# Performance work log

Measured on AMD Instinct MI355X. Metric: run time of the kernel, lower is better.

Reference implementation:

```python
import jax, jax.numpy as jnp
import numpy as np


def _lstm_selu(x, W, U, b):
    """Keras-semantics LSTM with activation='selu', return_sequences=True.
    x: [B, T, F]; W: [F, 4H]; U: [H, 4H]; b: [4H]. Gate order i, f, g, o.
    """
    B = x.shape[0]
    H = U.shape[0]
    # Precompute the input projection for all timesteps (one big GEMM).
    xz = jnp.einsum('btf,fg->btg', x, W) + b  # [B, T, 4H]

    def step(carry, xt):
        h, c = carry
        z = xt + h @ U  # [B, 4H]
        i, f, g, o = jnp.split(z, 4, axis=-1)
        i = jax.nn.sigmoid(i)
        f = jax.nn.sigmoid(f)
        g = jax.nn.selu(g)          # activation='selu' on candidate
        o = jax.nn.sigmoid(o)
        c = f * c + i * g
        h = o * jax.nn.selu(c)      # activation='selu' on cell output
        return (h, c), h

    h0 = jnp.zeros((B, H), x.dtype)
    c0 = jnp.zeros((B, H), x.dtype)
    (_, _), hs = jax.lax.scan(step, (h0, c0), jnp.swapaxes(xz, 0, 1))  # hs: [T, B, H]
    return jnp.swapaxes(hs, 0, 1)  # [B, T, H]


def setup_inputs() -> dict:
    key = jax.random.key(0)
    ks = jax.random.split(key, 6)
    B, T, F, H = 64, 2048, 64, 128
    s_in1 = 1.0 / np.sqrt(F)
    s_rec = 1.0 / np.sqrt(H)
    return {
        'x': jax.random.normal(ks[0], (B, T, F), dtype=jnp.float32),
        'W1': jax.random.normal(ks[1], (F, 4 * H), dtype=jnp.float32) * s_in1,
        'U1': jax.random.normal(ks[2], (H, 4 * H), dtype=jnp.float32) * s_rec,
        'b1': jnp.zeros((4 * H,), dtype=jnp.float32),
        'W2': jax.random.normal(ks[3], (H, 4 * H), dtype=jnp.float32) * s_rec,
        'U2': jax.random.normal(ks[4], (H, 4 * H), dtype=jnp.float32) * s_rec,
        'b2': jnp.zeros((4 * H,), dtype=jnp.float32),
    }


def reference(x, W1, U1, b1, W2, U2, b2):
    h1 = _lstm_selu(x, W1, U1, b1)   # layer 1, return_sequences=True
    h2 = _lstm_selu(h1, W2, U2, b2)  # layer 2 consumes layer-1 sequence
    return h2
```

## Files before the change

### kernel.cpp

```cpp
#include <hip/hip_runtime.h>
#include <hip/hip_bf16.h>

#define BATCH 64
#define SEQT  2048
#define FEAT  64
#define HID   128
#define G4    512
#define CHUNK 16
#define NCHUNK (SEQT / CHUNK)
#define XSP  68
#define H1P  136
#define XZP  516

using short8  = __attribute__((ext_vector_type(8))) short;
using floatx4 = __attribute__((ext_vector_type(4))) float;

__device__ __forceinline__ float sigmoidf_(float x) {
    return __builtin_amdgcn_rcpf(1.0f + __expf(-x));
}
__device__ __forceinline__ float seluf_(float x) {
    const float a = 1.6732632423543772f;
    const float s = 1.0507009873554805f;
    return x > 0.0f ? s * x : s * a * (__expf(x) - 1.0f);
}
__device__ __forceinline__ unsigned short f2bf_(float f) {
    unsigned u = __float_as_uint(f);
    u += 0x7FFFu + ((u >> 16) & 1u);
    return (unsigned short)(u >> 16);
}

__global__ __launch_bounds__(512)
__attribute__((amdgpu_waves_per_eu(2, 2)))
void fused_lstm(const float* __restrict__ x,
                const float* __restrict__ W1,
                const float* __restrict__ U1,
                const float* __restrict__ b1,
                const float* __restrict__ W2,
                const float* __restrict__ U2,
                const float* __restrict__ b2,
                unsigned long long* __restrict__ h1g,
                unsigned* __restrict__ flags,
                float* __restrict__ out) {
    const bool l2  = blockIdx.x >= BATCH;
    const int  b   = l2 ? ((int)blockIdx.x - BATCH) : (int)blockIdx.x;
    const int tid  = threadIdx.x;
    const int w    = tid >> 6;
    const int lane = tid & 63;
    const int c16  = lane & 15;
    const int quad = lane >> 4;
    const int j    = w * 16 + c16;

    __shared__ __align__(16) short hA[2][HID];
    __shared__ __align__(16) float xzbuf[CHUNK * XZP];
    __shared__ __align__(16) float xs[CHUNK * XSP];
    __shared__ __align__(16) short h1c[CHUNK * H1P];
    __shared__ __align__(16) short h1buf[CHUNK * HID];
    __shared__ __align__(16) float hbuf[CHUNK * HID];

    const float* U = l2 ? U2 : U1;
    short8 bfrag[4][4];
#pragma unroll
    for (int g = 0; g < 4; ++g) {
        const float* Ucol = U + (size_t)(g * 128 + j);
#pragma unroll
        for (int kc = 0; kc < 4; ++kc) {
            short8 v;
#pragma unroll
            for (int jj = 0; jj < 8; ++jj) {
                int k = kc * 32 + quad * 8 + jj;
                v[jj] = (short)f2bf_(Ucol[(size_t)k * G4]);
            }
            bfrag[g][kc] = v;
        }
    }

    const float* Wp = l2 ? W2 : W1;
    short8 wfrag[4][4];
#pragma unroll
    for (int g = 0; g < 4; ++g) {
        const float* Wcol = Wp + (size_t)(g * 128 + j);
#pragma unroll
        for (int kc = 0; kc < 4; ++kc) {
            short8 v;
            if (l2 || kc < 2) {
#pragma unroll
                for (int jj = 0; jj < 8; ++jj) {
                    int k = kc * 32 + quad * 8 + jj;
                    v[jj] = (short)f2bf_(Wcol[(size_t)k * G4]);
                }
            } else {
#pragma unroll
                for (int jj = 0; jj < 8; ++jj) v[jj] = 0;
            }
            wfrag[g][kc] = v;
        }
    }
    const float* bb = l2 ? b2 : b1;
    const float4 bias4 = make_float4(bb[j], bb[128 + j], bb[256 + j], bb[384 + j]);

    const float* xb = x + (size_t)b * SEQT * FEAT;
    if (!l2) {
        if (tid < 256) {
            float4 v = ((const float4*)xb)[tid];
            int t = tid >> 4, k4 = (tid & 15) << 2;
            *(float4*)&xs[t * XSP + k4] = v;
        }
    }
    if (tid < HID) hA[0][tid] = 0;
    float cst = 0.0f;
    floatx4 zero4 = {0.f, 0.f, 0.f, 0.f};
    __syncthreads();

    float*              out_b  = out + (size_t)b * SEQT * HID;
    unsigned long long* h1g_b  = h1g + (size_t)b * (SEQT * HID / 4);

    for (int c = 0; c < NCHUNK; ++c) {
        float4 pf;
        if (!l2) {
            if (c + 1 < NCHUNK && tid < 256)
                pf = ((const float4*)(xb + (size_t)(c + 1) * CHUNK * FEAT))[tid];
            short8 axf[2];
#pragma unroll
            for (int kc = 0; kc < 2; ++kc) {
                const float* p = &xs[c16 * XSP + kc * 32 + quad * 8];
                float4 f0 = *(const float4*)p;
                float4 f1 = *(const float4*)(p + 4);
                short8 v;
                v[0] = (short)f2bf_(f0.x); v[1] = (short)f2bf_(f0.y);
                v[2] = (short)f2bf_(f0.z); v[3] = (short)f2bf_(f0.w);
                v[4] = (short)f2bf_(f1.x); v[5] = (short)f2bf_(f1.y);
                v[6] = (short)f2bf_(f1.z); v[7] = (short)f2bf_(f1.w);
                axf[kc] = v;
            }
            floatx4 acc1[4];
#pragma unroll
            for (int g = 0; g < 4; ++g)
                acc1[g] = __builtin_amdgcn_mfma_f32_16x16x32_bf16(axf[0], wfrag[g][0], zero4, 0, 0, 0);
#pragma unroll
            for (int g = 0; g < 4; ++g)
                acc1[g] = __builtin_amdgcn_mfma_f32_16x16x32_bf16(axf[1], wfrag[g][1], acc1[g], 0, 0, 0);
#pragma unroll
            for (int r = 0; r < 4; ++r) {
                int s = quad * 4 + r;
                *(float4*)&xzbuf[s * XZP + j * 4] =
                    make_float4(acc1[0][r] + bias4.x, acc1[1][r] + bias4.y,
                                acc1[2][r] + bias4.z, acc1[3][r] + bias4.w);
            }
            __syncthreads();
        } else {
            if (tid == 0) {
                while (__hip_atomic_load(&flags[b], __ATOMIC_RELAXED,
                                         __HIP_MEMORY_SCOPE_AGENT) < (unsigned)(c + 1))
                    __builtin_amdgcn_s_sleep(8);
            }
            __syncthreads();
            {
                unsigned long long hv = __hip_atomic_load(
                    h1g_b + (size_t)c * 512 + tid, __ATOMIC_RELAXED, __HIP_MEMORY_SCOPE_AGENT);
                int t = tid >> 5, kg = tid & 31;
                *(unsigned long long*)&h1c[t * H1P + kg * 4] = hv;
            }
            __syncthreads();

            short8 af2[4];
#pragma unroll
            for (int kc = 0; kc < 4; ++kc)
                af2[kc] = *(const short8*)&h1c[c16 * H1P + kc * 32 + quad * 8];
            floatx4 acc2[4];
#pragma unroll
            for (int g = 0; g < 4; ++g)
                acc2[g] = __builtin_amdgcn_mfma_f32_16x16x32_bf16(af2[0], wfrag[g][0], zero4, 0, 0, 0);
#pragma unroll
            for (int kc = 1; kc < 4; ++kc)
#pragma unroll
                for (int g = 0; g < 4; ++g)
                    acc2[g] = __builtin_amdgcn_mfma_f32_16x16x32_bf16(af2[kc], wfrag[g][kc], acc2[g], 0, 0, 0);
#pragma unroll
            for (int r = 0; r < 4; ++r) {
                int s = quad * 4 + r;
                *(float4*)&xzbuf[s * XZP + j * 4] =
                    make_float4(acc2[0][r] + bias4.x, acc2[1][r] + bias4.y,
                                acc2[2][r] + bias4.z, acc2[3][r] + bias4.w);
            }
            __syncthreads();
        }

#pragma unroll 2
        for (int s = 0; s < CHUNK; ++s) {
            const short* hb = &hA[s & 1][0];
            short8 af[4];
#pragma unroll
            for (int kc = 0; kc < 4; ++kc)
                af[kc] = *(const short8*)&hb[kc * 32 + quad * 8];

            float4 xq = *(const float4*)&xzbuf[s * XZP + j * 4];

            floatx4 acc[4];
#pragma unroll
            for (int g = 0; g < 4; ++g)
                acc[g] = __builtin_amdgcn_mfma_f32_16x16x32_bf16(af[0], bfrag[g][0], zero4, 0, 0, 0);
#pragma unroll
            for (int kc = 1; kc < 4; ++kc)
#pragma unroll
                for (int g = 0; g < 4; ++g)
                    acc[g] = __builtin_amdgcn_mfma_f32_16x16x32_bf16(af[kc], bfrag[g][kc], acc[g], 0, 0, 0);

            float zi = acc[0][0] + xq.x;
            float zf = acc[1][0] + xq.y;
            float zg = acc[2][0] + xq.z;
            float zo = acc[3][0] + xq.w;
            float ig = sigmoidf_(zi);
            float fg = sigmoidf_(zf);
            float gg = seluf_(zg);
            float og = sigmoidf_(zo);
            cst = fg * cst + ig * gg;
            float h = og * seluf_(cst);

            if (lane < 16) {
                unsigned short hb16 = f2bf_(h);
                hA[(s + 1) & 1][j] = (short)hb16;
                if (l2) hbuf[s * HID + j] = h;
                else    h1buf[s * HID + j] = (short)hb16;
            }
            __syncthreads();
        }

        if (!l2) {
            unsigned long long hv = *(const unsigned long long*)&h1buf[tid * 4];
            __hip_atomic_store(h1g_b + (size_t)c * 512 + tid, hv,
                               __ATOMIC_RELAXED, __HIP_MEMORY_SCOPE_AGENT);
            if (c + 1 < NCHUNK && tid < 256) {
                int t = tid >> 4, k4 = (tid & 15) << 2;
                *(float4*)&xs[t * XSP + k4] = pf;
            }
            __syncthreads();
            if (tid == 0)
                __hip_atomic_store(&flags[b], (unsigned)(c + 1),
                                   __ATOMIC_RELAXED, __HIP_MEMORY_SCOPE_AGENT);
        } else {
            float4 hv = *(const float4*)&hbuf[tid * 4];
            *(float4*)&out_b[(size_t)c * CHUNK * HID + tid * 4] = hv;
        }
    }
}

extern "C" void kernel_launch(void* const* d_in, const int* in_sizes, int n_in,
                              void* d_out, int out_size, void* d_ws, size_t ws_size,
                              hipStream_t stream) {
    const float* x  = (const float*)d_in[0];
    const float* W1 = (const float*)d_in[1];
    const float* U1 = (const float*)d_in[2];
    const float* b1 = (const float*)d_in[3];
    const float* W2 = (const float*)d_in[4];
    const float* U2 = (const float*)d_in[5];
    const float* b2 = (const float*)d_in[6];
    float* out = (float*)d_out;

    const size_t BT       = (size_t)BATCH * SEQT;
    const size_t H1_BYTES = BT * HID * 2;

    unsigned long long* h1g   = (unsigned long long*)d_ws;
    unsigned*           flags = (unsigned*)((char*)d_ws + H1_BYTES);

    hipMemsetAsync(flags, 0, BATCH * sizeof(unsigned), stream);

    fused_lstm<<<dim3(2 * BATCH), dim3(512), 0, stream>>>(
        x, W1, U1, b1, W2, U2, b2, h1g, flags, out);
}
```

Measured before the change: 1.293 ms.

## Halve block to four waves, each owning two hidden-column groups with split-K MFMA chains

Cuts the workgroup from 8 to 4 waves so each wave computes 32 hidden columns, holding twice the U and W fragments in registers. The recurrent MFMA chain is split into two independent K-halves that are summed afterwards, which shortens the dependent chain and cuts the number of waves joining each per-step barrier. The spin-wait sleep is also shortened. The cost is a much higher register footprint, with possible spills at one wave per EU, and twice the gate math per thread on the serial critical path.

```diff
diff --git a/kernel.cpp b/kernel.cpp
--- a/kernel.cpp
+++ b/kernel.cpp
@@ -29,8 +29,8 @@
     return (unsigned short)(u >> 16);
 }
 
-__global__ __launch_bounds__(512)
-__attribute__((amdgpu_waves_per_eu(2, 2)))
+__global__ __launch_bounds__(256)
+__attribute__((amdgpu_waves_per_eu(1, 1)))
 void fused_lstm(const float* __restrict__ x,
                 const float* __restrict__ W1,
                 const float* __restrict__ U1,
@@ -48,7 +48,8 @@
     const int lane = tid & 63;
     const int c16  = lane & 15;
     const int quad = lane >> 4;
-    const int j    = w * 16 + c16;
+    const int j0   = w * 32 + c16;
+    const int j1   = j0 + 16;
 
     __shared__ __align__(16) short hA[2][HID];
     __shared__ __align__(16) float xzbuf[CHUNK * XZP];
@@ -58,68 +59,68 @@
     __shared__ __align__(16) float hbuf[CHUNK * HID];
 
     const float* U = l2 ? U2 : U1;
-    short8 bfrag[4][4];
-#pragma unroll
-    for (int g = 0; g < 4; ++g) {
-        const float* Ucol = U + (size_t)(g * 128 + j);
-#pragma unroll
-        for (int kc = 0; kc < 4; ++kc) {
-            short8 v;
-#pragma unroll
-            for (int jj = 0; jj < 8; ++jj) {
-                int k = kc * 32 + quad * 8 + jj;
-                v[jj] = (short)f2bf_(Ucol[(size_t)k * G4]);
-            }
-            bfrag[g][kc] = v;
-        }
-    }
-
-    const float* Wp = l2 ? W2 : W1;
-    short8 wfrag[4][4];
-#pragma unroll
-    for (int g = 0; g < 4; ++g) {
-        const float* Wcol = Wp + (size_t)(g * 128 + j);
-#pragma unroll
-        for (int kc = 0; kc < 4; ++kc) {
-            short8 v;
-            if (l2 || kc < 2) {
+    short8 bfrag[4][4][2];
+#pragma unroll
+    for (int g = 0; g < 4; ++g)
+#pragma unroll
+        for (int grp = 0; grp < 2; ++grp) {
+            const float* Ucol = U + (size_t)(g * 128 + w * 32 + grp * 16 + c16);
+#pragma unroll
+            for (int kc = 0; kc < 4; ++kc) {
+                short8 v;
 #pragma unroll
                 for (int jj = 0; jj < 8; ++jj) {
                     int k = kc * 32 + quad * 8 + jj;
-                    v[jj] = (short)f2bf_(Wcol[(size_t)k * G4]);
-                }
-            } else {
-#pragma unroll
-                for (int jj = 0; jj < 8; ++jj) v[jj] = 0;
-            }
-            wfrag[g][kc] = v;
-        }
-    }
+                    v[jj] = (short)f2bf_(Ucol[(size_t)k * G4]);
+                }
+                bfrag[kc][g][grp] = v;
+            }
+        }
+
+    const float* Wp = l2 ? W2 : W1;
+    const int KCW = l2 ? 4 : 2;
+    short8 wfrag[4][4][2];
+#pragma unroll
+    for (int g = 0; g < 4; ++g)
+#pragma unroll
+        for (int grp = 0; grp < 2; ++grp) {
+            const float* Wcol = Wp + (size_t)(g * 128 + w * 32 + grp * 16 + c16);
+#pragma unroll
+            for (int kc = 0; kc < 4; ++kc) {
+                if (kc < KCW) {
+                    short8 v;
+#pragma unroll
+                    for (int jj = 0; jj < 8; ++jj) {
+                        int k = kc * 32 + quad * 8 + jj;
+                        v[jj] = (short)f2bf_(Wcol[(size_t)k * G4]);
+                    }
+                    wfrag[kc][g][grp] = v;
+                }
+            }
+        }
     const float* bb = l2 ? b2 : b1;
-    const float4 bias4 = make_float4(bb[j], bb[128 + j], bb[256 + j], bb[384 + j]);
+    const float4 biasA = make_float4(bb[j0], bb[128 + j0], bb[256 + j0], bb[384 + j0]);
+    const float4 biasB = make_float4(bb[j1], bb[128 + j1], bb[256 + j1], bb[384 + j1]);
 
     const float* xb = x + (size_t)b * SEQT * FEAT;
     if (!l2) {
-        if (tid < 256) {
-            float4 v = ((const float4*)xb)[tid];
-            int t = tid >> 4, k4 = (tid & 15) << 2;
-            *(float4*)&xs[t * XSP + k4] = v;
-        }
+        float4 v = ((const float4*)xb)[tid];
+        *(float4*)&xs[(tid >> 4) * XSP + ((tid & 15) << 2)] = v;
     }
     if (tid < HID) hA[0][tid] = 0;
-    float cst = 0.0f;
+    float cst0 = 0.0f, cst1 = 0.0f;
     floatx4 zero4 = {0.f, 0.f, 0.f, 0.f};
     __syncthreads();
 
-    float*              out_b  = out + (size_t)b * SEQT * HID;
-    unsigned long long* h1g_b  = h1g + (size_t)b * (SEQT * HID / 4);
+    float*              out_b = out + (size_t)b * SEQT * HID;
+    unsigned long long* h1g_b = h1g + (size_t)b * (SEQT * HID / 4);
 
     for (int c = 0; c < NCHUNK; ++c) {
         float4 pf;
         if (!l2) {
-            if (c + 1 < NCHUNK && tid < 256)
+            if (c + 1 < NCHUNK)
                 pf = ((const float4*)(xb + (size_t)(c + 1) * CHUNK * FEAT))[tid];
-            short8 axf[2];
+            short8 ax[2];
 #pragma unroll
             for (int kc = 0; kc < 2; ++kc) {
                 const float* p = &xs[c16 * XSP + kc * 32 + quad * 8];
@@ -130,57 +131,66 @@
                 v[2] = (short)f2bf_(f0.z); v[3] = (short)f2bf_(f0.w);
                 v[4] = (short)f2bf_(f1.x); v[5] = (short)f2bf_(f1.y);
                 v[6] = (short)f2bf_(f1.z); v[7] = (short)f2bf_(f1.w);
-                axf[kc] = v;
-            }
-            floatx4 acc1[4];
+                ax[kc] = v;
+            }
+            floatx4 acc1[4][2];
 #pragma unroll
             for (int g = 0; g < 4; ++g)
-                acc1[g] = __builtin_amdgcn_mfma_f32_16x16x32_bf16(axf[0], wfrag[g][0], zero4, 0, 0, 0);
-#pragma unroll
-            for (int g = 0; g < 4; ++g)
-                acc1[g] = __builtin_amdgcn_mfma_f32_16x16x32_bf16(axf[1], wfrag[g][1], acc1[g], 0, 0, 0);
+#pragma unroll
+                for (int grp = 0; grp < 2; ++grp) {
+                    floatx4 t = __builtin_amdgcn_mfma_f32_16x16x32_bf16(ax[0], wfrag[0][g][grp], zero4, 0, 0, 0);
+                    acc1[g][grp] = __builtin_amdgcn_mfma_f32_16x16x32_bf16(ax[1], wfrag[1][g][grp], t, 0, 0, 0);
+                }
 #pragma unroll
             for (int r = 0; r < 4; ++r) {
-                int s = quad * 4 + r;
-                *(float4*)&xzbuf[s * XZP + j * 4] =
-                    make_float4(acc1[0][r] + bias4.x, acc1[1][r] + bias4.y,
-                                acc1[2][r] + bias4.z, acc1[3][r] + bias4.w);
+                int srow = quad * 4 + r;
+                *(float4*)&xzbuf[srow * XZP + j0 * 4] =
+                    make_float4(acc1[0][0][r] + biasA.x, acc1[1][0][r] + biasA.y,
+                                acc1[2][0][r] + biasA.z, acc1[3][0][r] + biasA.w);
+                *(float4*)&xzbuf[srow * XZP + j1 * 4] =
+                    make_float4(acc1[0][1][r] + biasB.x, acc1[1][1][r] + biasB.y,
+                                acc1[2][1][r] + biasB.z, acc1[3][1][r] + biasB.w);
             }
             __syncthreads();
         } else {
             if (tid == 0) {
                 while (__hip_atomic_load(&flags[b], __ATOMIC_RELAXED,
                                          __HIP_MEMORY_SCOPE_AGENT) < (unsigned)(c + 1))
-                    __builtin_amdgcn_s_sleep(8);
-            }
-            __syncthreads();
-            {
+                    __builtin_amdgcn_s_sleep(2);
+            }
+            __syncthreads();
+#pragma unroll
+            for (int i = 0; i < 2; ++i) {
+                int idx = tid + i * 256;
                 unsigned long long hv = __hip_atomic_load(
-                    h1g_b + (size_t)c * 512 + tid, __ATOMIC_RELAXED, __HIP_MEMORY_SCOPE_AGENT);
-                int t = tid >> 5, kg = tid & 31;
-                *(unsigned long long*)&h1c[t * H1P + kg * 4] = hv;
-            }
-            __syncthreads();
-
-            short8 af2[4];
+                    h1g_b + (size_t)c * 512 + idx, __ATOMIC_RELAXED, __HIP_MEMORY_SCOPE_AGENT);
+                *(unsigned long long*)&h1c[(idx >> 5) * H1P + (idx & 31) * 4] = hv;
+            }
+            __syncthreads();
+
+            short8 ah[4];
 #pragma unroll
             for (int kc = 0; kc < 4; ++kc)
-                af2[kc] = *(const short8*)&h1c[c16 * H1P + kc * 32 + quad * 8];
-            floatx4 acc2[4];
+                ah[kc] = *(const short8*)&h1c[c16 * H1P + kc * 32 + quad * 8];
+            floatx4 acc2[4][2];
 #pragma unroll
             for (int g = 0; g < 4; ++g)
-                acc2[g] = __builtin_amdgcn_mfma_f32_16x16x32_bf16(af2[0], wfrag[g][0], zero4, 0, 0, 0);
-#pragma unroll
-            for (int kc = 1; kc < 4; ++kc)
-#pragma unroll
-                for (int g = 0; g < 4; ++g)
-                    acc2[g] = __builtin_amdgcn_mfma_f32_16x16x32_bf16(af2[kc], wfrag[g][kc], acc2[g], 0, 0, 0);
+#pragma unroll
+                for (int grp = 0; grp < 2; ++grp) {
+                    floatx4 t = __builtin_amdgcn_mfma_f32_16x16x32_bf16(ah[0], wfrag[0][g][grp], zero4, 0, 0, 0);
+                    t = __builtin_amdgcn_mfma_f32_16x16x32_bf16(ah[1], wfrag[1][g][grp], t, 0, 0, 0);
+                    t = __builtin_amdgcn_mfma_f32_16x16x32_bf16(ah[2], wfrag[2][g][grp], t, 0, 0, 0);
+                    acc2[g][grp] = __builtin_amdgcn_mfma_f32_16x16x32_bf16(ah[3], wfrag[3][g][grp], t, 0, 0, 0);
+                }
 #pragma unroll
             for (int r = 0; r < 4; ++r) {
-                int s = quad * 4 + r;
-                *(float4*)&xzbuf[s * XZP + j * 4] =
-                    make_float4(acc2[0][r] + bias4.x, acc2[1][r] + bias4.y,
-                                acc2[2][r] + bias4.z, acc2[3][r] + bias4.w);
+                int srow = quad * 4 + r;
+                *(float4*)&xzbuf[srow * XZP + j0 * 4] =
+                    make_float4(acc2[0][0][r] + biasA.x, acc2[1][0][r] + biasA.y,
+                                acc2[2][0][r] + biasA.z, acc2[3][0][r] + biasA.w);
+                *(float4*)&xzbuf[srow * XZP + j1 * 4] =
+                    make_float4(acc2[0][1][r] + biasB.x, acc2[1][1][r] + biasB.y,
+                                acc2[2][1][r] + biasB.z, acc2[3][1][r] + biasB.w);
             }
             __syncthreads();
         }
@@ -192,54 +202,76 @@
 #pragma unroll
             for (int kc = 0; kc < 4; ++kc)
                 af[kc] = *(const short8*)&hb[kc * 32 + quad * 8];
-
-            float4 xq = *(const float4*)&xzbuf[s * XZP + j * 4];
-
-            floatx4 acc[4];
+            float4 xqA = *(const float4*)&xzbuf[s * XZP + j0 * 4];
+            float4 xqB = *(const float4*)&xzbuf[s * XZP + j1 * 4];
+
+            floatx4 accA[4][2], accB[4][2];
 #pragma unroll
             for (int g = 0; g < 4; ++g)
-                acc[g] = __builtin_amdgcn_mfma_f32_16x16x32_bf16(af[0], bfrag[g][0], zero4, 0, 0, 0);
-#pragma unroll
-            for (int kc = 1; kc < 4; ++kc)
-#pragma unroll
-                for (int g = 0; g < 4; ++g)
-                    acc[g] = __builtin_amdgcn_mfma_f32_16x16x32_bf16(af[kc], bfrag[g][kc], acc[g], 0, 0, 0);
-
-            float zi = acc[0][0] + xq.x;
-            float zf = acc[1][0] + xq.y;
-            float zg = acc[2][0] + xq.z;
-            float zo = acc[3][0] + xq.w;
-            float ig = sigmoidf_(zi);
-            float fg = sigmoidf_(zf);
-            float gg = seluf_(zg);
-            float og = sigmoidf_(zo);
-            cst = fg * cst + ig * gg;
-            float h = og * seluf_(cst);
-
-            if (lane < 16) {
-                unsigned short hb16 = f2bf_(h);
-                hA[(s + 1) & 1][j] = (short)hb16;
-                if (l2) hbuf[s * HID + j] = h;
-                else    h1buf[s * HID + j] = (short)hb16;
+#pragma unroll
+                for (int grp = 0; grp < 2; ++grp) {
+                    floatx4 t0 = __builtin_amdgcn_mfma_f32_16x16x32_bf16(af[0], bfrag[0][g][grp], zero4, 0, 0, 0);
+                    accA[g][grp] = __builtin_amdgcn_mfma_f32_16x16x32_bf16(af[1], bfrag[1][g][grp], t0, 0, 0, 0);
+                    floatx4 t1 = __builtin_amdgcn_mfma_f32_16x16x32_bf16(af[2], bfrag[2][g][grp], zero4, 0, 0, 0);
+                    accB[g][grp] = __builtin_amdgcn_mfma_f32_16x16x32_bf16(af[3], bfrag[3][g][grp], t1, 0, 0, 0);
+                }
+
+            float h0, h1f;
+            unsigned short h0b, h1b;
+            {
+                float zi = accA[0][0][0] + accB[0][0][0] + xqA.x;
+                float zf = accA[1][0][0] + accB[1][0][0] + xqA.y;
+                float zg = accA[2][0][0] + accB[2][0][0] + xqA.z;
+                float zo = accA[3][0][0] + accB[3][0][0] + xqA.w;
+                float ig = sigmoidf_(zi), fg = sigmoidf_(zf);
+                float gg = seluf_(zg),   og = sigmoidf_(zo);
+                cst0 = fg * cst0 + ig * gg;
+                h0 = og * seluf_(cst0);
+                h0b = f2bf_(h0);
+            }
+            {
+                float zi = accA[0][1][0] + accB[0][1][0] + xqB.x;
+                float zf = accA[1][1][0] + accB[1][1][0] + xqB.y;
+                float zg = accA[2][1][0] + accB[2][1][0] + xqB.z;
+                float zo = accA[3][1][0] + accB[3][1][0] + xqB.w;
+                float ig = sigmoidf_(zi), fg = sigmoidf_(zf);
+                float gg = seluf_(zg),   og = sigmoidf_(zo);
+                cst1 = fg * cst1 + ig * gg;
+                h1f = og * seluf_(cst1);
+                h1b = f2bf_(h1f);
+            }
+
+            if (lane < 32) {
+                int col = w * 32 + lane;
+                unsigned short hv = (lane < 16) ? h0b : h1b;
+                hA[(s + 1) & 1][col] = (short)hv;
+                if (l2) hbuf[s * HID + col] = (lane < 16) ? h0 : h1f;
+                else    h1buf[s * HID + col] = (short)hv;
             }
             __syncthreads();
         }
 
         if (!l2) {
-            unsigned long long hv = *(const unsigned long long*)&h1buf[tid * 4];
-            __hip_atomic_store(h1g_b + (size_t)c * 512 + tid, hv,
-                               __ATOMIC_RELAXED, __HIP_MEMORY_SCOPE_AGENT);
-            if (c + 1 < NCHUNK && tid < 256) {
-                int t = tid >> 4, k4 = (tid & 15) << 2;
-                *(float4*)&xs[t * XSP + k4] = pf;
-            }
+#pragma unroll
+            for (int i = 0; i < 2; ++i) {
+                int idx = tid + i * 256;
+                unsigned long long hv = *(const unsigned long long*)&h1buf[idx * 4];
+                __hip_atomic_store(h1g_b + (size_t)c * 512 + idx, hv,
+                                   __ATOMIC_RELAXED, __HIP_MEMORY_SCOPE_AGENT);
+            }
+            if (c + 1 < NCHUNK)
+                *(float4*)&xs[(tid >> 4) * XSP + ((tid & 15) << 2)] = pf;
             __syncthreads();
             if (tid == 0)
                 __hip_atomic_store(&flags[b], (unsigned)(c + 1),
                                    __ATOMIC_RELAXED, __HIP_MEMORY_SCOPE_AGENT);
         } else {
-            float4 hv = *(const float4*)&hbuf[tid * 4];
-            *(float4*)&out_b[(size_t)c * CHUNK * HID + tid * 4] = hv;
+#pragma unroll
+            for (int i = 0; i < 2; ++i) {
+                int idx = tid + i * 256;
+                *(float4*)&out_b[(size_t)c * CHUNK * HID + idx * 4] =
+                    *(const float4*)&hbuf[idx * 4];
+            }
         }
     }
 }
@@ -264,6 +296,6 @@
 
     hipMemsetAsync(flags, 0, BATCH * sizeof(unsigned), stream);
 
-    fused_lstm<<<dim3(2 * BATCH), dim3(512), 0, stream>>>(
+    fused_lstm<<<dim3(2 * BATCH), dim3(256), 0, stream>>>(
         x, W1, U1, b1, W2, U2, b2, h1g, flags, out);
 }
```

New measurement: 1.736 ms. 1.34x slower.

## Fuse both LSTM layers into one 1024-thread block per batch with skewed chunks

Applied to the files above, without the earlier changes.

Rather than running layer-1 and layer-2 in separate blocks that talk through global memory with flag spin-waits, each block now has 16 waves. Waves 0-7 run layer 1 and waves 8-15 run layer 2, one chunk behind, and they hand off h1 through a double-buffered shared-memory tile. Input-projection weights are pre-converted to bf16 fragments by a small prep kernel and read from global memory rather than held in registers, which frees registers for the 1024-thread launch. The intent is to remove the global handoff, the atomics and the polling latency. The cost is that both layers now share one barrier per timestep, layer 2's output is written per step, and only 64 blocks run.

```diff
diff --git a/kernel.cpp b/kernel.cpp
--- a/kernel.cpp
+++ b/kernel.cpp
@@ -15,6 +15,8 @@
 using short8  = __attribute__((ext_vector_type(8))) short;
 using floatx4 = __attribute__((ext_vector_type(4))) float;
 
+#define BAR_LGKM() asm volatile("s_waitcnt lgkmcnt(0)\n\ts_barrier" ::: "memory")
+
 __device__ __forceinline__ float sigmoidf_(float x) {
     return __builtin_amdgcn_rcpf(1.0f + __expf(-x));
 }
@@ -29,35 +31,53 @@
     return (unsigned short)(u >> 16);
 }
 
-__global__ __launch_bounds__(512)
-__attribute__((amdgpu_waves_per_eu(2, 2)))
+__global__ __launch_bounds__(256) void prep_weights(const float* __restrict__ W1,
+                                                    const float* __restrict__ W2,
+                                                    unsigned short* __restrict__ wsf) {
+    int idx = blockIdx.x * 256 + threadIdx.x;
+    int KC, fi, obase;
+    const float* src;
+    if (idx < 4096) { KC = 2; src = W1; fi = idx;        obase = 0; }
+    else            { KC = 4; src = W2; fi = idx - 4096; obase = 4096 * 8; }
+    int g  = fi & 3;
+    int r  = fi >> 2;
+    int kc = r % KC;
+    int p  = r / KC;
+    int q  = p & 3;
+    int j  = p >> 2;
+    short8 v;
+#pragma unroll
+    for (int jj = 0; jj < 8; ++jj)
+        v[jj] = (short)f2bf_(src[(size_t)(kc * 32 + q * 8 + jj) * G4 + g * 128 + j]);
+    *(short8*)&wsf[obase + fi * 8] = v;
+}
+
+__global__ __launch_bounds__(1024)
 void fused_lstm(const float* __restrict__ x,
-                const float* __restrict__ W1,
                 const float* __restrict__ U1,
                 const float* __restrict__ b1,
-                const float* __restrict__ W2,
                 const float* __restrict__ U2,
                 const float* __restrict__ b2,
-                unsigned long long* __restrict__ h1g,
-                unsigned* __restrict__ flags,
+                const unsigned short* __restrict__ wsf,
                 float* __restrict__ out) {
-    const bool l2  = blockIdx.x >= BATCH;
-    const int  b   = l2 ? ((int)blockIdx.x - BATCH) : (int)blockIdx.x;
+    const int  b   = (int)blockIdx.x;
     const int tid  = threadIdx.x;
     const int w    = tid >> 6;
+    const bool l2w = w >= 8;
+    const int  wl  = w & 7;
     const int lane = tid & 63;
     const int c16  = lane & 15;
     const int quad = lane >> 4;
-    const int j    = w * 16 + c16;
-
-    __shared__ __align__(16) short hA[2][HID];
-    __shared__ __align__(16) float xzbuf[CHUNK * XZP];
+    const int j    = wl * 16 + c16;
+
+    __shared__ __align__(16) short hA1[2][HID];
+    __shared__ __align__(16) short hA2[2][HID];
+    __shared__ __align__(16) float xz1[CHUNK * XZP];
+    __shared__ __align__(16) float xz2[CHUNK * XZP];
     __shared__ __align__(16) float xs[CHUNK * XSP];
-    __shared__ __align__(16) short h1c[CHUNK * H1P];
-    __shared__ __align__(16) short h1buf[CHUNK * HID];
-    __shared__ __align__(16) float hbuf[CHUNK * HID];
-
-    const float* U = l2 ? U2 : U1;
+    __shared__ __align__(16) short h1x[2][CHUNK * H1P];
+
+    const float* U = l2w ? U2 : U1;
     short8 bfrag[4][4];
 #pragma unroll
     for (int g = 0; g < 4; ++g) {
@@ -70,177 +90,115 @@
                 int k = kc * 32 + quad * 8 + jj;
                 v[jj] = (short)f2bf_(Ucol[(size_t)k * G4]);
             }
-            bfrag[g][kc] = v;
+            bfrag[kc][g] = v;
         }
     }
-
-    const float* Wp = l2 ? W2 : W1;
-    short8 wfrag[4][4];
-#pragma unroll
-    for (int g = 0; g < 4; ++g) {
-        const float* Wcol = Wp + (size_t)(g * 128 + j);
-#pragma unroll
-        for (int kc = 0; kc < 4; ++kc) {
-            short8 v;
-            if (l2 || kc < 2) {
-#pragma unroll
-                for (int jj = 0; jj < 8; ++jj) {
-                    int k = kc * 32 + quad * 8 + jj;
-                    v[jj] = (short)f2bf_(Wcol[(size_t)k * G4]);
-                }
-            } else {
-#pragma unroll
-                for (int jj = 0; jj < 8; ++jj) v[jj] = 0;
-            }
-            wfrag[g][kc] = v;
-        }
+    const float* bb = l2w ? b2 : b1;
+    const float4 bias4 = make_float4(bb[j], bb[128 + j], bb[256 + j], bb[384 + j]);
+
+    const int KC = l2w ? 4 : 2;
+    const short8* wtb = (const short8*)(wsf + (l2w ? 32768 : 0)
+                                            + (size_t)(j * 4 + quad) * KC * 32);
+
+    const float* xb    = x + (size_t)b * SEQT * FEAT;
+    float*       out_b = out + (size_t)b * SEQT * HID;
+
+    if (!l2w && tid < 256) {
+        float4 v = ((const float4*)xb)[tid];
+        *(float4*)&xs[(tid >> 4) * XSP + ((tid & 15) << 2)] = v;
     }
-    const float* bb = l2 ? b2 : b1;
-    const float4 bias4 = make_float4(bb[j], bb[128 + j], bb[256 + j], bb[384 + j]);
-
-    const float* xb = x + (size_t)b * SEQT * FEAT;
-    if (!l2) {
-        if (tid < 256) {
-            float4 v = ((const float4*)xb)[tid];
-            int t = tid >> 4, k4 = (tid & 15) << 2;
-            *(float4*)&xs[t * XSP + k4] = v;
-        }
-    }
-    if (tid < HID) hA[0][tid] = 0;
+    if (tid < HID) hA1[0][tid] = 0;
+    else if (tid < 2 * HID) hA2[0][tid - HID] = 0;
     float cst = 0.0f;
     floatx4 zero4 = {0.f, 0.f, 0.f, 0.f};
     __syncthreads();
 
-    float*              out_b  = out + (size_t)b * SEQT * HID;
-    unsigned long long* h1g_b  = h1g + (size_t)b * (SEQT * HID / 4);
-
-    for (int c = 0; c < NCHUNK; ++c) {
+    short (*hAp)[HID] = l2w ? hA2 : hA1;
+    float* myxz       = l2w ? xz2 : xz1;
+
+    for (int c = 0; c <= NCHUNK; ++c) {
+        const bool act = l2w ? (c >= 1) : (c < NCHUNK);
         float4 pf;
-        if (!l2) {
-            if (c + 1 < NCHUNK && tid < 256)
-                pf = ((const float4*)(xb + (size_t)(c + 1) * CHUNK * FEAT))[tid];
-            short8 axf[2];
-#pragma unroll
-            for (int kc = 0; kc < 2; ++kc) {
-                const float* p = &xs[c16 * XSP + kc * 32 + quad * 8];
-                float4 f0 = *(const float4*)p;
-                float4 f1 = *(const float4*)(p + 4);
-                short8 v;
-                v[0] = (short)f2bf_(f0.x); v[1] = (short)f2bf_(f0.y);
-                v[2] = (short)f2bf_(f0.z); v[3] = (short)f2bf_(f0.w);
-                v[4] = (short)f2bf_(f1.x); v[5] = (short)f2bf_(f1.y);
-                v[6] = (short)f2bf_(f1.z); v[7] = (short)f2bf_(f1.w);
-                axf[kc] = v;
-            }
-            floatx4 acc1[4];
-#pragma unroll
-            for (int g = 0; g < 4; ++g)
-                acc1[g] = __builtin_amdgcn_mfma_f32_16x16x32_bf16(axf[0], wfrag[g][0], zero4, 0, 0, 0);
-#pragma unroll
-            for (int g = 0; g < 4; ++g)
-                acc1[g] = __builtin_amdgcn_mfma_f32_16x16x32_bf16(axf[1], wfrag[g][1], acc1[g], 0, 0, 0);
+        if (!l2w && c + 1 < NCHUNK && tid < 256)
+            pf = ((const float4*)(xb + (size_t)(c + 1) * CHUNK * FEAT))[tid];
+
+        if (act) {
+            floatx4 accp[4] = {zero4, zero4, zero4, zero4};
+            for (int kc = 0; kc < KC; ++kc) {
+                short8 aop;
+                if (!l2w) {
+                    const float* p = &xs[c16 * XSP + kc * 32 + quad * 8];
+                    float4 f0 = *(const float4*)p;
+                    float4 f1 = *(const float4*)(p + 4);
+                    aop[0] = (short)f2bf_(f0.x); aop[1] = (short)f2bf_(f0.y);
+                    aop[2] = (short)f2bf_(f0.z); aop[3] = (short)f2bf_(f0.w);
+                    aop[4] = (short)f2bf_(f1.x); aop[5] = (short)f2bf_(f1.y);
+                    aop[6] = (short)f2bf_(f1.z); aop[7] = (short)f2bf_(f1.w);
+                } else {
+                    aop = *(const short8*)&h1x[(c + 1) & 1][c16 * H1P + kc * 32 + quad * 8];
+                }
+                short8 w0 = wtb[kc * 4 + 0], w1 = wtb[kc * 4 + 1];
+                short8 w2 = wtb[kc * 4 + 2], w3 = wtb[kc * 4 + 3];
+                accp[0] = __builtin_amdgcn_mfma_f32_16x16x32_bf16(aop, w0, accp[0], 0, 0, 0);
+                accp[1] = __builtin_amdgcn_mfma_f32_16x16x32_bf16(aop, w1, accp[1], 0, 0, 0);
+                accp[2] = __builtin_amdgcn_mfma_f32_16x16x32_bf16(aop, w2, accp[2], 0, 0, 0);
+                accp[3] = __builtin_amdgcn_mfma_f32_16x16x32_bf16(aop, w3, accp[3], 0, 0, 0);
+            }
 #pragma unroll
             for (int r = 0; r < 4; ++r) {
-                int s = quad * 4 + r;
-                *(float4*)&xzbuf[s * XZP + j * 4] =
-                    make_float4(acc1[0][r] + bias4.x, acc1[1][r] + bias4.y,
-                                acc1[2][r] + bias4.z, acc1[3][r] + bias4.w);
-            }
-            __syncthreads();
-        } else {
-            if (tid == 0) {
-                while (__hip_atomic_load(&flags[b], __ATOMIC_RELAXED,
-                                         __HIP_MEMORY_SCOPE_AGENT) < (unsigned)(c + 1))
-                    __builtin_amdgcn_s_sleep(8);
-            }
-            __syncthreads();
-            {
-                unsigned long long hv = __hip_atomic_load(
-                    h1g_b + (size_t)c * 512 + tid, __ATOMIC_RELAXED, __HIP_MEMORY_SCOPE_AGENT);
-                int t = tid >> 5, kg = tid & 31;
-                *(unsigned long long*)&h1c[t * H1P + kg * 4] = hv;
-            }
-            __syncthreads();
-
-            short8 af2[4];
-#pragma unroll
-            for (int kc = 0; kc < 4; ++kc)
-                af2[kc] = *(const short8*)&h1c[c16 * H1P + kc * 32 + quad * 8];
-            floatx4 acc2[4];
-#pragma unroll
-            for (int g = 0; g < 4; ++g)
-                acc2[g] = __builtin_amdgcn_mfma_f32_16x16x32_bf16(af2[0], wfrag[g][0], zero4, 0, 0, 0);
-#pragma unroll
-            for (int kc = 1; kc < 4; ++kc)
+                int srow = quad * 4 + r;
+                *(float4*)&myxz[srow * XZP + j * 4] =
+                    make_float4(accp[0][r] + bias4.x, accp[1][r] + bias4.y,
+                                accp[2][r] + bias4.z, accp[3][r] + bias4.w);
+            }
+        }
+        BAR_LGKM();
+
+        for (int s = 0; s < CHUNK; ++s) {
+            if (act) {
+                const short* hb = &hAp[s & 1][0];
+                short8 af[4];
+#pragma unroll
+                for (int kc = 0; kc < 4; ++kc)
+                    af[kc] = *(const short8*)&hb[kc * 32 + quad * 8];
+                float4 xq = *(const float4*)&myxz[s * XZP + j * 4];
+
+                floatx4 acc[4];
 #pragma unroll
                 for (int g = 0; g < 4; ++g)
-                    acc2[g] = __builtin_amdgcn_mfma_f32_16x16x32_bf16(af2[kc], wfrag[g][kc], acc2[g], 0, 0, 0);
-#pragma unroll
-            for (int r = 0; r < 4; ++r) {
-                int s = quad * 4 + r;
-                *(float4*)&xzbuf[s * XZP + j * 4] =
-                    make_float4(acc2[0][r] + bias4.x, acc2[1][r] + bias4.y,
-                                acc2[2][r] + bias4.z, acc2[3][r] + bias4.w);
-            }
-            __syncthreads();
+                    acc[g] = __builtin_amdgcn_mfma_f32_16x16x32_bf16(af[0], bfrag[0][g], zero4, 0, 0, 0);
+#pragma unroll
+                for (int kc = 1; kc < 4; ++kc)
+#pragma unroll
+                    for (int g = 0; g < 4; ++g)
+                        acc[g] = __builtin_amdgcn_mfma_f32_16x16x32_bf16(af[kc], bfrag[kc][g], acc[g], 0, 0, 0);
+
+                float zi = acc[0][0] + xq.x;
+                float zf = acc[1][0] + xq.y;
+                float zg = acc[2][0] + xq.z;
+                float zo = acc[3][0] + xq.w;
+                float ig = sigmoidf_(zi), fg = sigmoidf_(zf);
+                float gg = seluf_(zg),   og = sigmoidf_(zo);
+                cst = fg * cst + ig * gg;
+                float h = og * seluf_(cst);
+
+                if (lane < 16) {
+                    unsigned short h16 = f2bf_(h);
+                    if (!l2w) {
+                        hA1[(s + 1) & 1][j] = (short)h16;
+                        h1x[c & 1][s * H1P + j] = (short)h16;
+                    } else {
+                        hA2[(s + 1) & 1][j] = (short)h16;
+                        out_b[(size_t)((c - 1) * CHUNK + s) * HID + j] = h;
+                    }
+                }
+            }
+            BAR_LGKM();
         }
 
-#pragma unroll 2
-        for (int s = 0; s < CHUNK; ++s) {
-            const short* hb = &hA[s & 1][0];
-            short8 af[4];
-#pragma unroll
-            for (int kc = 0; kc < 4; ++kc)
-                af[kc] = *(const short8*)&hb[kc * 32 + quad * 8];
-
-            float4 xq = *(const float4*)&xzbuf[s * XZP + j * 4];
-
-            floatx4 acc[4];
-#pragma unroll
-            for (int g = 0; g < 4; ++g)
-                acc[g] = __builtin_amdgcn_mfma_f32_16x16x32_bf16(af[0], bfrag[g][0], zero4, 0, 0, 0);
-#pragma unroll
-            for (int kc = 1; kc < 4; ++kc)
-#pragma unroll
-                for (int g = 0; g < 4; ++g)
-                    acc[g] = __builtin_amdgcn_mfma_f32_16x16x32_bf16(af[kc], bfrag[g][kc], acc[g], 0, 0, 0);
-
-            float zi = acc[0][0] + xq.x;
-            float zf = acc[1][0] + xq.y;
-            float zg = acc[2][0] + xq.z;
-            float zo = acc[3][0] + xq.w;
-            float ig = sigmoidf_(zi);
-            float fg = sigmoidf_(zf);
-            float gg = seluf_(zg);
-            float og = sigmoidf_(zo);
-            cst = fg * cst + ig * gg;
-            float h = og * seluf_(cst);
-
-            if (lane < 16) {
-                unsigned short hb16 = f2bf_(h);
-                hA[(s + 1) & 1][j] = (short)hb16;
-                if (l2) hbuf[s * HID + j] = h;
-                else    h1buf[s * HID + j] = (short)hb16;
-            }
-            __syncthreads();
-        }
-
-        if (!l2) {
-            unsigned long long hv = *(const unsigned long long*)&h1buf[tid * 4];
-            __hip_atomic_store(h1g_b + (size_t)c * 512 + tid, hv,
-                               __ATOMIC_RELAXED, __HIP_MEMORY_SCOPE_AGENT);
-            if (c + 1 < NCHUNK && tid < 256) {
-                int t = tid >> 4, k4 = (tid & 15) << 2;
-                *(float4*)&xs[t * XSP + k4] = pf;
-            }
-            __syncthreads();
-            if (tid == 0)
-                __hip_atomic_store(&flags[b], (unsigned)(c + 1),
-                                   __ATOMIC_RELAXED, __HIP_MEMORY_SCOPE_AGENT);
-        } else {
-            float4 hv = *(const float4*)&hbuf[tid * 4];
-            *(float4*)&out_b[(size_t)c * CHUNK * HID + tid * 4] = hv;
-        }
+        if (!l2w && c + 1 < NCHUNK && tid < 256)
+            *(float4*)&xs[(tid >> 4) * XSP + ((tid & 15) << 2)] = pf;
+        BAR_LGKM();
     }
 }
 
@@ -256,14 +214,10 @@
     const float* b2 = (const float*)d_in[6];
     float* out = (float*)d_out;
 
-    const size_t BT       = (size_t)BATCH * SEQT;
-    const size_t H1_BYTES = BT * HID * 2;
-
-    unsigned long long* h1g   = (unsigned long long*)d_ws;
-    unsigned*           flags = (unsigned*)((char*)d_ws + H1_BYTES);
-
-    hipMemsetAsync(flags, 0, BATCH * sizeof(unsigned), stream);
-
-    fused_lstm<<<dim3(2 * BATCH), dim3(512), 0, stream>>>(
-        x, W1, U1, b1, W2, U2, b2, h1g, flags, out);
-}
+    unsigned short* wsf = (unsigned short*)d_ws;
+
+    prep_weights<<<dim3(48), dim3(256), 0, stream>>>(W1, W2, wsf);
+
+    fused_lstm<<<dim3(BATCH), dim3(1024), 0, stream>>>(
+        x, U1, b1, U2, b2, wsf, out);
+}
```

Result: slower. 2.458 ms (+90.1%).
